# Optimization experiments

Measured on AMD Instinct MI355X. Metric: run time of the kernel, lower is better.

Reference implementation:

```python
import jax, jax.numpy as jnp
import numpy as np

NQ = 16  # nqubits
BATCH = 256

def _ry(t):
    # t: (...,) real angles -> (..., 2, 2) complex64 Ry(t)
    c = jnp.cos(t / 2).astype(jnp.complex64)
    s = jnp.sin(t / 2).astype(jnp.complex64)
    return jnp.stack([jnp.stack([c, -s], -1), jnp.stack([s, c], -1)], -2)

def _rz(t):
    # diag(e^{-i t/2}, e^{i t/2})
    e0 = jnp.exp(-0.5j * t.astype(jnp.complex64))
    e1 = jnp.exp(0.5j * t.astype(jnp.complex64))
    z = jnp.zeros_like(e0)
    return jnp.stack([jnp.stack([e0, z], -1), jnp.stack([z, e1], -1)], -2)

def _apply_1q(st, g, w):
    # st: (B, 2^n) complex, g: (2,2) or (B,2,2); wire w (0 = most significant, matching kron order)
    B = st.shape[0]
    x = st.reshape(B, 2 ** w, 2, -1)
    if g.ndim == 3:
        x = jnp.einsum('iab,ilbr->ilar', g, x)
    else:
        x = jnp.einsum('ab,ilbr->ilar', g, x)
    return x.reshape(B, -1)

def _apply_cnot(st, c, t, n):
    # CNOT(control=c, target=t): flip target bit where control bit == 1
    B = st.shape[0]
    x = st.reshape((B,) + (2,) * n)
    c_ax = c + 1
    ctrl0 = jnp.take(x, 0, axis=c_ax)
    ctrl1 = jnp.take(x, 1, axis=c_ax)
    t_ax = t + 1 if t < c else t  # target axis index after removing control axis
    ctrl1 = jnp.flip(ctrl1, axis=t_ax)  # flip along size-2 axis == Pauli-X
    x = jnp.stack([ctrl0, ctrl1], axis=c_ax)
    return x.reshape(B, -1)

def _yzy(st, w3, n):
    # per-qubit Ry(a) Rz(b) Ry(c); params laid out (n, 3) applied in order a, b, c
    p = w3.reshape(n, 3)
    g = jnp.einsum('nab,nbc,ncd->nad', _ry(p[:, 2]), _rz(p[:, 1]), _ry(p[:, 0]))
    for i in range(n):
        st = _apply_1q(st, g[i], i)
    return st

def _ring(st, step, n):
    # ring_of_cnot (step=1) / ring_of_cnot2 (step=2)
    for i in range(n):
        st = _apply_cnot(st, i, (i + step) % n, n)
    return st

def _forward(inputs, weight):
    B, n = inputs.shape
    # |0...0> initial state, batched
    st = jnp.zeros((B, 2 ** n), jnp.complex64).at[:, 0].set(1.0)
    # PauliEncoding with pauli='Y': Ry(inputs[:, i]) on wire i (batched gate)
    enc = _ry(inputs)  # (B, n, 2, 2)
    for i in range(n):
        st = _apply_1q(st, enc[:, i], i)
    # BasicEntangleLayer x2 = YZY + ring_of_cnot
    st = _yzy(st, weight[0 * n:3 * n], n); st = _ring(st, 1, n)
    st = _yzy(st, weight[3 * n:6 * n], n); st = _ring(st, 1, n)
    # YZY, ring_of_cnot2, YZY, ring_of_cnot2, YZY
    st = _yzy(st, weight[6 * n:9 * n], n); st = _ring(st, 2, n)
    st = _yzy(st, weight[9 * n:12 * n], n); st = _ring(st, 2, n)
    st = _yzy(st, weight[12 * n:15 * n], n)
    # <Z_i> = sum_probs(bit_i=0) - sum_probs(bit_i=1); output scaled by 4 as in original
    probs = st.real ** 2 + st.imag ** 2  # (B, 2^n) real
    z = []
    for i in range(n):
        p = probs.reshape(B, 2 ** i, 2, -1)
        z.append((p[:, :, 0, :] - p[:, :, 1, :]).sum(axis=(1, 2)))
    return jnp.stack(z, axis=1) * 4.0  # (B, n)

def setup_inputs() -> dict:
    key = jax.random.key(0)
    k1, k2 = jax.random.split(key)
    inputs = jax.random.uniform(k1, (BATCH, NQ), jnp.float32, 0.0, 2.0 * np.pi)
    weight = jax.random.uniform(k2, (15 * NQ,), jnp.float32, 0.0, 2.0 * np.pi)
    return {"inputs": inputs, "weight": weight}

def reference(inputs, weight):
    return _forward(inputs, weight)
```

## Files before the change

kernel.cpp:

```cpp
#include <hip/hip_runtime.h>
#include <hip/hip_fp16.h>
#include <utility>
#include <type_traits>


constexpr int NSR  = 96;
constexpr int NGRR = 24;
constexpr int NGL  = 8;
constexpr int NG   = 32;

struct M16 { unsigned r[16]; };

constexpr M16 ident() { M16 m{}; for (int i = 0; i < 16; ++i) m.r[i] = 1u << i; return m; }

constexpr M16 ringm(int s) {
  M16 m = ident();
  for (int i = 15; i >= 0; --i) {
    int pc = 15 - i;
    int pt = 15 - ((i + s) & 15);
    m.r[pt] ^= m.r[pc];
  }
  return m;
}

constexpr M16 mmul(M16 A, M16 B) {
  M16 C{};
  for (int p = 0; p < 16; ++p) {
    unsigned v = 0;
    for (int q = 0; q < 16; ++q) if ((A.r[p] >> q) & 1u) v ^= B.r[q];
    C.r[p] = v;
  }
  return C;
}

constexpr M16 minv(M16 A) {
  M16 I = ident();
  for (int col = 0; col < 16; ++col) {
    int piv = -1;
    for (int row = col; row < 16; ++row) if ((A.r[row] >> col) & 1u) { piv = row; break; }
    unsigned t = A.r[piv]; A.r[piv] = A.r[col]; A.r[col] = t;
    t = I.r[piv]; I.r[piv] = I.r[col]; I.r[col] = t;
    for (int row = 0; row < 16; ++row)
      if (row != col && ((A.r[row] >> col) & 1u)) { A.r[row] ^= A.r[col]; I.r[row] ^= I.r[col]; }
  }
  return I;
}

constexpr bool meq(M16 a, M16 b) { for (int i = 0; i < 16; ++i) if (a.r[i] != b.r[i]) return false; return true; }
constexpr unsigned colmask(M16 P, int b) { unsigned m = 0; for (int p = 0; p < 16; ++p) m |= ((P.r[p] >> b) & 1u) << p; return m; }
constexpr int popc16(unsigned x) { int c = 0; for (int i = 0; i < 16; ++i) c += (x >> i) & 1; return c; }
constexpr int topbit_pow(unsigned x) { int b = 0; for (int i = 0; i < 16; ++i) if ((x >> i) & 1) b = i; return 1 << b; }

struct Tables { unsigned gm[64]; unsigned gc[64]; unsigned meas[16]; };

constexpr Tables make_tables() {
  Tables T{};
  M16 R1 = ringm(1), R2 = ringm(2);
  M16 P0 = R1;
  M16 P1 = mmul(R1, R1);
  M16 P2 = mmul(P1, R2);
  M16 P3 = mmul(P2, R2);
  M16 P[4] = { P0, P1, P2, P3 };
  for (int k = 0; k < 4; ++k) {
    M16 A = minv(P[k]);
    for (int b = 0; b < 16; ++b) {
      T.gm[k * 16 + b] = colmask(P[k], b);
      T.gc[k * 16 + b] = A.r[b];
    }
  }
  M16 A5 = minv(P[3]);
  for (int w = 0; w < 16; ++w) T.meas[w] = A5.r[15 - w];
  return T;
}

constexpr Tables TB = make_tables();

constexpr bool check_tables() {
  for (int g = 0; g < 64; ++g) if ((popc16(TB.gm[g] & TB.gc[g]) & 1) != 1) return false;
  if (!meq(mmul(ringm(1), minv(ringm(1))), ident())) return false;
  if (!meq(mmul(ringm(2), minv(ringm(2))), ident())) return false;
  return true;
}
static_assert(check_tables(), "GF(2) table inconsistency");
static_assert(sizeof(__half2) == 4, "half2 size");

template<int N, int I = 0, typename F>
__device__ __forceinline__ void sfor(F&& f) {
  if constexpr (I < N) {
    f(std::integral_constant<int, I>{});
    sfor<N, I + 1>(static_cast<F&&>(f));
  }
}

__device__ __forceinline__ int h2i(__half2 v) { return __builtin_bit_cast(int, v); }
__device__ __forceinline__ __half2 i2h(int v) { return __builtin_bit_cast(__half2, v); }
__device__ __forceinline__ unsigned h2u(__half2 v) { return __builtin_bit_cast(unsigned, v); }
__device__ __forceinline__ __half2 u2h(unsigned v) { return __builtin_bit_cast(__half2, v); }

__device__ __forceinline__ void upd2(__half2& x0r, __half2& x1r,
                                     __half2 xp0_, __half2 xp1_,
                                     __half2 c0_, __half2 c1a_, __half2 c1b_,
                                     __half2 c2a_, __half2 c2b_, __half2 c3_) {
  const unsigned x0 = h2u(x0r), x1 = h2u(x1r), xp0 = h2u(xp0_), xp1 = h2u(xp1_);
  const unsigned c0 = h2u(c0_), c1a = h2u(c1a_), c1b = h2u(c1b_),
                 c2a = h2u(c2a_), c2b = h2u(c2b_), c3 = h2u(c3_);
  unsigned y0, y1;
  asm("v_pk_mul_f16 %0, %2, %3\n\t"
      "v_pk_mul_f16 %1, %2, %4\n\t"
      "v_pk_fma_f16 %0, %5, %3, %0 op_sel:[0,1,0] op_sel_hi:[1,0,1]\n\t"
      "v_pk_fma_f16 %1, %6, %4, %1 op_sel:[0,1,0] op_sel_hi:[1,0,1]\n\t"
      "v_pk_fma_f16 %0, %7, %9, %0\n\t"
      "v_pk_fma_f16 %1, %8, %10, %1\n\t"
      "v_pk_fma_f16 %0, %11, %9, %0 op_sel:[0,1,0] op_sel_hi:[1,0,1]\n\t"
      "v_pk_fma_f16 %1, %11, %10, %1 op_sel:[0,1,0] op_sel_hi:[1,0,1]"
      : "=&v"(y0), "=&v"(y1)
      : "v"(c0), "v"(x0), "v"(x1), "v"(c1a), "v"(c1b),
        "v"(c2a), "v"(c2b), "v"(xp0), "v"(xp1), "v"(c3));
  x0r = u2h(y0); x1r = u2h(y1);
}

template<int lx>
__device__ __forceinline__ __half2 pget(__half2 v) {
  if constexpr (lx == 0) return v;
  else return i2h(__shfl_xor(h2i(v), lx, 64));
}

__device__ __forceinline__ void su2_coeffs(float a, float b, float c,
                                           float& are, float& aim, float& bre, float& bim) {
  float sapc, capc, samc, camc, sb, cb;
  __sincosf((a + c) * 0.5f, &sapc, &capc);
  __sincosf((a - c) * 0.5f, &samc, &camc);
  __sincosf(b * 0.5f, &sb, &cb);
  are = cb * capc;
  aim = -sb * camc;
  bre = cb * sapc;
  bim = sb * samc;
}

__device__ __forceinline__ unsigned pkh2(float lo, float hi) {
  return h2u(__floats2half2_rn(lo, hi));
}

__device__ __forceinline__ float2 cmulf(float2 a, float vr, float vi) {
  return make_float2(a.x * vr - a.y * vi, a.x * vi + a.y * vr);
}

template<int G>
__device__ __forceinline__ void vg_load(const __half2 (&S)[NSR], const uint4* sg4,
                                        unsigned tid, __half2 (&a)[4]) {
  if constexpr (G < NGRR) {
    a[0] = S[4*G]; a[1] = S[4*G+1]; a[2] = S[4*G+2]; a[3] = S[4*G+3];
  } else {
    const uint4 v = sg4[(G - NGRR) * 512 + tid];
    a[0] = u2h(v.x); a[1] = u2h(v.y); a[2] = u2h(v.z); a[3] = u2h(v.w);
  }
}
template<int G>
__device__ __forceinline__ void vg_store(__half2 (&S)[NSR], uint4* sg4,
                                         unsigned tid, const __half2 (&a)[4]) {
  if constexpr (G < NGRR) {
    S[4*G] = a[0]; S[4*G+1] = a[1]; S[4*G+2] = a[2]; S[4*G+3] = a[3];
  } else {
    sg4[(G - NGRR) * 512 + tid] = make_uint4(h2u(a[0]), h2u(a[1]), h2u(a[2]), h2u(a[3]));
  }
}
template<int G>
__device__ __forceinline__ uint4 vg_pack(const __half2 (&S)[NSR], const uint4* sg4, unsigned tid) {
  if constexpr (G < NGRR)
    return make_uint4(h2u(S[4*G]), h2u(S[4*G+1]), h2u(S[4*G+2]), h2u(S[4*G+3]));
  else
    return sg4[(G - NGRR) * 512 + tid];
}

template<int G, int me, unsigned cm>
__device__ __forceinline__ void vg_upd(__half2 (&S)[NSR], uint4* sg4, unsigned tid, uint4 pv,
                                       __half2 c0, __half2 c1p, __half2 c1n,
                                       __half2 c2p, __half2 c2n, __half2 c3) {
  const unsigned q[4] = { pv.x, pv.y, pv.z, pv.w };
  __half2 a[4]; vg_load<G>(S, sg4, tid, a);
  constexpr int t0 = popc16(cm & (unsigned)(4*G+0)) & 1;
  constexpr int t1 = popc16(cm & (unsigned)(4*G+1)) & 1;
  constexpr int t2 = popc16(cm & (unsigned)(4*G+2)) & 1;
  constexpr int t3 = popc16(cm & (unsigned)(4*G+3)) & 1;
  upd2(a[0], a[1], u2h(q[0^me]), u2h(q[1^me]),
       c0, t0?c1n:c1p, t1?c1n:c1p, t0?c2n:c2p, t1?c2n:c2p, c3);
  upd2(a[2], a[3], u2h(q[2^me]), u2h(q[3^me]),
       c0, t2?c1n:c1p, t3?c1n:c1p, t2?c2n:c2p, t3?c2n:c2p, c3);
  vg_store<G>(S, sg4, tid, a);
}

template<int G>
__device__ __forceinline__ void apply_gate(__half2 (&S)[NSR], unsigned tid,
                                           const uint4* __restrict__ ctabg,
                                           uint4* sg4, uint4* xbuf4) {
  constexpr unsigned m  = TB.gm[G];
  constexpr unsigned c  = TB.gc[G];
  constexpr unsigned mL = m & 127u;
  constexpr unsigned mT = m >> 7;
  constexpr unsigned mW = m >> 13;

  const uint4 cc = ctabg[G];
  const unsigned fm = (__popc((c >> 7) & tid) & 1u) ? 0x80008000u : 0u;
  const unsigned c1u = cc.y ^ fm, c2u = cc.z ^ fm;
  const __half2 c0 = u2h(cc.x), c3 = u2h(cc.w);
  const __half2 c1p = u2h(c1u), c1n = u2h(c1u ^ 0x80008000u);
  const __half2 c2p = u2h(c2u), c2n = u2h(c2u ^ 0x80008000u);

  if constexpr (mW == 0u) {
    constexpr int lx = (int)mT;
    if constexpr (mL == 0u) {
      sfor<NG>([&](auto gg) {
        constexpr int g = decltype(gg)::value;
        __half2 a[4]; vg_load<g>(S, sg4, tid, a);
        const __half2 p0 = pget<lx>(a[0]), p1 = pget<lx>(a[1]);
        const __half2 p2 = pget<lx>(a[2]), p3 = pget<lx>(a[3]);
        constexpr int t0 = popc16(c & (unsigned)(4*g+0)) & 1;
        constexpr int t1 = popc16(c & (unsigned)(4*g+1)) & 1;
        constexpr int t2 = popc16(c & (unsigned)(4*g+2)) & 1;
        constexpr int t3 = popc16(c & (unsigned)(4*g+3)) & 1;
        upd2(a[0], a[1], p0, p1, c0, t0?c1n:c1p, t1?c1n:c1p, t0?c2n:c2p, t1?c2n:c2p, c3);
        upd2(a[2], a[3], p2, p3, c0, t2?c1n:c1p, t3?c1n:c1p, t2?c2n:c2p, t3?c2n:c2p, c3);
        vg_store<g>(S, sg4, tid, a);
      });
    } else if constexpr ((mL >> 2) == 0u) {
      constexpr int tb = topbit_pow(mL);
      sfor<NG>([&](auto gg) {
        constexpr int g = decltype(gg)::value;
        __half2 a[4]; vg_load<g>(S, sg4, tid, a);
        sfor<4>([&](auto ee) {
          constexpr int e = decltype(ee)::value;
          if constexpr ((e & tb) == 0) {
            constexpr int e1 = e ^ (int)mL;
            constexpr int t0 = popc16(c & (unsigned)(4*g+e)) & 1;
            constexpr int t1 = popc16(c & (unsigned)(4*g+e1)) & 1;
            const __half2 x0 = a[e], x1 = a[e1];
            upd2(a[e], a[e1], pget<lx>(x1), pget<lx>(x0),
                 c0, t0?c1n:c1p, t1?c1n:c1p, t0?c2n:c2p, t1?c2n:c2p, c3);
          }
        });
        vg_store<g>(S, sg4, tid, a);
      });
    } else {
      constexpr int hg = (int)(mL >> 2);
      constexpr int tb = topbit_pow((unsigned)hg);
      constexpr int me = (int)(mL & 3u);
      sfor<NG>([&](auto ga_) {
        constexpr int gA = decltype(ga_)::value;
        if constexpr ((gA & tb) == 0) {
          constexpr int gB = gA ^ hg;
          __half2 a[4], b4[4];
          vg_load<gA>(S, sg4, tid, a); vg_load<gB>(S, sg4, tid, b4);
          sfor<4>([&](auto ee) {
            constexpr int e  = decltype(ee)::value;
            constexpr int e2 = e ^ me;
            constexpr int t0 = popc16(c & (unsigned)(4*gA+e)) & 1;
            constexpr int t1 = popc16(c & (unsigned)(4*gB+e2)) & 1;
            const __half2 x0 = a[e], x1 = b4[e2];
            upd2(a[e], b4[e2], pget<lx>(x1), pget<lx>(x0),
                 c0, t0?c1n:c1p, t1?c1n:c1p, t0?c2n:c2p, t1?c2n:c2p, c3);
          });
          vg_store<gA>(S, sg4, tid, a); vg_store<gB>(S, sg4, tid, b4);
        }
      });
    }
  } else {
    const unsigned ptid = tid ^ (unsigned)mT;
    constexpr unsigned hG = mL >> 2;
    constexpr int      me = (int)(mL & 3u);
    if constexpr (hG == 0u) {
      sfor<4>([&](auto rr) {
        constexpr int r = decltype(rr)::value;
        sfor<8>([&](auto kk) {
          constexpr int k = decltype(kk)::value;
          xbuf4[tid * 9u + (unsigned)k] = vg_pack<r * 8 + k>(S, sg4, tid);
        });
        __syncthreads();
        sfor<8>([&](auto kk) {
          constexpr int k = decltype(kk)::value;
          const uint4 pv = xbuf4[ptid * 9u + (unsigned)k];
          vg_upd<r * 8 + k, me, c>(S, sg4, tid, pv, c0, c1p, c1n, c2p, c2n, c3);
        });
        __syncthreads();
      });
    } else {
      constexpr int tbG = topbit_pow(hG);
      sfor<4>([&](auto rr) {
        constexpr int r = decltype(rr)::value;
        sfor<4>([&](auto kk) {
          constexpr int k  = decltype(kk)::value;
          constexpr int i  = r * 4 + k;
          constexpr int gA = ((i & ~(tbG - 1)) << 1) | (i & (tbG - 1));
          constexpr int gB = gA ^ (int)hG;
          xbuf4[tid * 9u + (unsigned)k]       = vg_pack<gA>(S, sg4, tid);
          xbuf4[tid * 9u + (unsigned)(4 + k)] = vg_pack<gB>(S, sg4, tid);
        });
        __syncthreads();
        sfor<4>([&](auto kk) {
          constexpr int k  = decltype(kk)::value;
          constexpr int i  = r * 4 + k;
          constexpr int gA = ((i & ~(tbG - 1)) << 1) | (i & (tbG - 1));
          constexpr int gB = gA ^ (int)hG;
          const uint4 pvB = xbuf4[ptid * 9u + (unsigned)(4 + k)];
          const uint4 pvA = xbuf4[ptid * 9u + (unsigned)k];
          vg_upd<gA, me, c>(S, sg4, tid, pvB, c0, c1p, c1n, c2p, c2n, c3);
          vg_upd<gB, me, c>(S, sg4, tid, pvA, c0, c1p, c1n, c2p, c2n, c3);
        });
        __syncthreads();
      });
    }
  }
}

__global__ void ctab_build(const float* __restrict__ weight, uint4* __restrict__ ctabg) {
  const int g = (int)threadIdx.x;
  const int k = g >> 4;
  const int bb = g & 15;
  const int w = 15 - bb;
  const int base = 48 * (k + 1) + 3 * w;
  float are, aim, bre, bim;
  su2_coeffs(weight[base], weight[base + 1], weight[base + 2], are, aim, bre, bim);
  ctabg[g] = make_uint4(pkh2(are, are), pkh2(-aim, aim),
                        pkh2(-bre, -bre), pkh2(-bim, bim));
}

__global__ __attribute__((amdgpu_flat_work_group_size(512, 512)))
void qcir_kernel(const float* __restrict__ inputs, const float* __restrict__ weight,
                 float* __restrict__ out, const uint4* __restrict__ ctabg) {
  __shared__ uint4  sg4[NGL * 512];
  __shared__ uint4  xbuf4[512 * 9];
  __shared__ float4 itab[16];
  __shared__ float  red[8 * 16];

  const unsigned tid = threadIdx.x;
  const unsigned b   = blockIdx.x;

  if (tid < 16) {
    const int w = (int)tid;
    const float a = weight[3 * w] + inputs[b * 16 + w];
    float are, aim, bre, bim;
    su2_coeffs(a, weight[3 * w + 1], weight[3 * w + 2], are, aim, bre, bim);
    itab[w] = make_float4(are, aim, bre, bim);
  }
  __syncthreads();

  __half2 S[NSR];
  float2 P = make_float2(1.f, 0.f);
#pragma unroll
  for (int p = 7; p <= 15; ++p) {
    const int bit = (int)(tid >> (p - 7)) & 1;
    const float4 t = itab[15 - p];
    P = cmulf(P, bit ? t.z : t.x, bit ? t.w : t.y);
  }
  sfor<16>([&](auto hh) {
    constexpr int h = decltype(hh)::value;
    float2 ph = P;
    sfor<4>([&](auto qq) {
      constexpr int q   = decltype(qq)::value;
      constexpr int bit = (h >> q) & 1;
      const float4 t = itab[12 - q];
      if constexpr (bit) ph = cmulf(ph, t.z, t.w); else ph = cmulf(ph, t.x, t.y);
    });
    if constexpr (h < 12) {
      sfor<8>([&](auto ll) {
        constexpr int l = decltype(ll)::value;
        float2 pl = ph;
        sfor<3>([&](auto qq) {
          constexpr int q   = decltype(qq)::value;
          constexpr int bit = (l >> q) & 1;
          const float4 t = itab[15 - q];
          if constexpr (bit) pl = cmulf(pl, t.z, t.w); else pl = cmulf(pl, t.x, t.y);
        });
        S[h * 8 + l] = __floats2half2_rn(pl.x, pl.y);
      });
    } else {
      __half2 a0[4], a1[4];
      sfor<8>([&](auto ll) {
        constexpr int l = decltype(ll)::value;
        float2 pl = ph;
        sfor<3>([&](auto qq) {
          constexpr int q   = decltype(qq)::value;
          constexpr int bit = (l >> q) & 1;
          const float4 t = itab[15 - q];
          if constexpr (bit) pl = cmulf(pl, t.z, t.w); else pl = cmulf(pl, t.x, t.y);
        });
        const __half2 v = __floats2half2_rn(pl.x, pl.y);
        if constexpr (l < 4) a0[l] = v; else a1[l - 4] = v;
      });
      sg4[(2 * (h - 12)) * 512 + tid]     = make_uint4(h2u(a0[0]), h2u(a0[1]), h2u(a0[2]), h2u(a0[3]));
      sg4[(2 * (h - 12) + 1) * 512 + tid] = make_uint4(h2u(a1[0]), h2u(a1[1]), h2u(a1[2]), h2u(a1[3]));
    }
  });
  __syncthreads();

  sfor<64>([&](auto gg) { apply_gate<decltype(gg)::value>(S, tid, ctabg, sg4, xbuf4); });

  sfor<2>([&](auto hf_) {
    constexpr int hf = decltype(hf_)::value;
    float acc[8];
    sfor<8>([&](auto ww) { acc[decltype(ww)::value] = 0.f; });
    sfor<NSR>([&](auto ll) {
      constexpr int L = decltype(ll)::value;
      const float re = __low2float(S[L]);
      const float im = __high2float(S[L]);
      const float p = re * re + im * im;
      sfor<8>([&](auto w8) {
        constexpr int w = hf * 8 + decltype(w8)::value;
        constexpr int t = popc16(TB.meas[w] & 127u & (unsigned)L) & 1;
        if constexpr (t) acc[decltype(w8)::value] -= p; else acc[decltype(w8)::value] += p;
      });
    });
    sfor<NGL>([&](auto gg) {
      constexpr int g = decltype(gg)::value;
      const uint4 v = sg4[g * 512 + tid];
      const unsigned q[4] = { v.x, v.y, v.z, v.w };
      sfor<4>([&](auto ee) {
        constexpr int e = decltype(ee)::value;
        constexpr int L = NSR + g * 4 + e;
        const __half2 av = u2h(q[e]);
        const float re = __low2float(av);
        const float im = __high2float(av);
        const float p = re * re + im * im;
        sfor<8>([&](auto w8) {
          constexpr int w = hf * 8 + decltype(w8)::value;
          constexpr int t = popc16(TB.meas[w] & 127u & (unsigned)L) & 1;
          if constexpr (t) acc[decltype(w8)::value] -= p; else acc[decltype(w8)::value] += p;
        });
      });
    });
    sfor<8>([&](auto w8) {
      constexpr int w = hf * 8 + decltype(w8)::value;
      const unsigned fw = __popc((TB.meas[w] >> 7) & tid) & 1u;
      float z = fw ? -acc[decltype(w8)::value] : acc[decltype(w8)::value];
#pragma unroll
      for (int d = 1; d < 64; d <<= 1) z += __shfl_xor(z, d, 64);
      if ((tid & 63u) == 0u) red[(tid >> 6) * 16 + w] = z;
    });
  });
  __syncthreads();
  if (tid < 16) {
    float s = 0.f;
#pragma unroll
    for (int v = 0; v < 8; ++v) s += red[v * 16 + tid];
    out[b * 16 + tid] = 4.f * s;
  }
}

extern "C" void kernel_launch(void* const* d_in, const int* in_sizes, int n_in,
                              void* d_out, int out_size, void* d_ws, size_t ws_size,
                              hipStream_t stream) {
  const float* inputs = (const float*)d_in[0];
  const float* weight = (const float*)d_in[1];
  float* out = (float*)d_out;
  const int B = in_sizes[0] / 16;
  uint4* ctabg = reinterpret_cast<uint4*>(d_ws);
  ctab_build<<<1, 64, 0, stream>>>(weight, ctabg);
  qcir_kernel<<<B, 512, 0, stream>>>(inputs, weight, out, ctabg);
}
```

Before: 279.0 us.

## Permute qubit-to-bit assignment at compile time to minimize cross-thread gate exchanges

Result: no change. 282.5 us (+1.3%).

```diff
diff --git a/kernel.cpp b/kernel.cpp
--- a/kernel.cpp
+++ b/kernel.cpp
@@ -73,7 +73,67 @@
   return T;
 }
 
-constexpr Tables TB = make_tables();
+constexpr Tables TB_RAW = make_tables();
+
+struct Assign { int a[16]; };
+
+constexpr Assign make_assign() {
+  int bx = 13, by = 14, bz = 15, bestw = 1 << 30;
+  for (int x = 0; x < 16; ++x)
+    for (int y = x + 1; y < 16; ++y)
+      for (int z = y + 1; z < 16; ++z) {
+        const unsigned W = (1u << x) | (1u << y) | (1u << z);
+        int cnt = 0;
+        for (int g = 0; g < 64; ++g) if (TB_RAW.gm[g] & W) ++cnt;
+        if (cnt < bestw) { bestw = cnt; bx = x; by = y; bz = z; }
+      }
+  const unsigned Wf = (1u << bx) | (1u << by) | (1u << bz);
+  int rem[13] = {}; int nr = 0;
+  for (int b = 0; b < 16; ++b) if (!((Wf >> b) & 1)) rem[nr++] = b;
+  unsigned bestL = 0; int bestc = -1;
+  for (unsigned s = 0; s < (1u << 13); ++s) {
+    if (popc16(s) != 7) continue;
+    unsigned Lm = 0;
+    for (int i = 0; i < 13; ++i) if ((s >> i) & 1) Lm |= 1u << rem[i];
+    int cnt = 0;
+    for (int g = 0; g < 64; ++g) if ((TB_RAW.gm[g] & ~Lm) == 0) ++cnt;
+    if (cnt > bestc) { bestc = cnt; bestL = Lm; }
+  }
+  Assign A{}; int pl = 0, pn = 7, pw = 13;
+  for (int b = 0; b < 16; ++b) {
+    if ((bestL >> b) & 1)      A.a[pl++] = b;
+    else if ((Wf >> b) & 1)    A.a[pw++] = b;
+    else                       A.a[pn++] = b;
+  }
+  return A;
+}
+
+constexpr Assign AS = make_assign();
+
+constexpr bool assign_ok() {
+  unsigned seen = 0;
+  for (int p = 0; p < 16; ++p) {
+    if (AS.a[p] < 0 || AS.a[p] > 15) return false;
+    seen |= 1u << AS.a[p];
+  }
+  return seen == 0xFFFFu;
+}
+static_assert(assign_ok(), "ASSIGN not a permutation");
+
+constexpr unsigned permute_mask(unsigned m) {
+  unsigned r = 0;
+  for (int p = 0; p < 16; ++p) r |= ((m >> AS.a[p]) & 1u) << p;
+  return r;
+}
+
+constexpr Tables permute_tables() {
+  Tables T{};
+  for (int g = 0; g < 64; ++g) { T.gm[g] = permute_mask(TB_RAW.gm[g]); T.gc[g] = permute_mask(TB_RAW.gc[g]); }
+  for (int w = 0; w < 16; ++w) T.meas[w] = permute_mask(TB_RAW.meas[w]);
+  return T;
+}
+
+constexpr Tables TB = permute_tables();
 
 constexpr bool check_tables() {
   for (int g = 0; g < 64; ++g) if ((popc16(TB.gm[g] & TB.gc[g]) & 1) != 1) return false;
@@ -345,19 +405,19 @@
 
   __half2 S[NSR];
   float2 P = make_float2(1.f, 0.f);
-#pragma unroll
-  for (int p = 7; p <= 15; ++p) {
+  sfor<9>([&](auto pp) {
+    constexpr int p = 7 + decltype(pp)::value;
     const int bit = (int)(tid >> (p - 7)) & 1;
-    const float4 t = itab[15 - p];
+    const float4 t = itab[15 - AS.a[p]];
     P = cmulf(P, bit ? t.z : t.x, bit ? t.w : t.y);
-  }
+  });
   sfor<16>([&](auto hh) {
     constexpr int h = decltype(hh)::value;
     float2 ph = P;
     sfor<4>([&](auto qq) {
       constexpr int q   = decltype(qq)::value;
       constexpr int bit = (h >> q) & 1;
-      const float4 t = itab[12 - q];
+      const float4 t = itab[15 - AS.a[3 + q]];
       if constexpr (bit) ph = cmulf(ph, t.z, t.w); else ph = cmulf(ph, t.x, t.y);
     });
     if constexpr (h < 12) {
@@ -367,7 +427,7 @@
         sfor<3>([&](auto qq) {
           constexpr int q   = decltype(qq)::value;
           constexpr int bit = (l >> q) & 1;
-          const float4 t = itab[15 - q];
+          const float4 t = itab[15 - AS.a[q]];
           if constexpr (bit) pl = cmulf(pl, t.z, t.w); else pl = cmulf(pl, t.x, t.y);
         });
         S[h * 8 + l] = __floats2half2_rn(pl.x, pl.y);
@@ -380,7 +440,7 @@
         sfor<3>([&](auto qq) {
           constexpr int q   = decltype(qq)::value;
           constexpr int bit = (l >> q) & 1;
-          const float4 t = itab[15 - q];
+          const float4 t = itab[15 - AS.a[q]];
           if constexpr (bit) pl = cmulf(pl, t.z, t.w); else pl = cmulf(pl, t.x, t.y);
         });
         const __half2 v = __floats2half2_rn(pl.x, pl.y);
```
